# Kernel tuning notes

Measured on AMD Instinct MI355X. Metric: run time of the kernel, lower is better.

The kernel has to match this reference:

```python
import jax, jax.numpy as jnp
import numpy as np

# dims
B, C, H, W = 2, 256, 128, 256
P, G = 9, 8            # num_pts, num_groups
GC = C // G            # group_channels


def setup_inputs() -> dict:
    key = jax.random.key(0)
    ks = jax.random.split(key, 8)
    s = 0.02
    return {
        "feats1": jax.random.normal(ks[0], (B, C, H, W), jnp.float32),
        "feats2": jax.random.normal(ks[1], (B, C, H, W), jnp.float32),
        "anchor_points": jax.random.uniform(ks[2], (B, H * W, 2), jnp.float32),
        "norm1_g": jnp.ones((C,), jnp.float32), "norm1_b": jnp.zeros((C,), jnp.float32),
        "norm2_g": jnp.ones((C,), jnp.float32), "norm2_b": jnp.zeros((C,), jnp.float32),
        "Wv": jax.random.normal(ks[3], (C, C), jnp.float32) * s, "bv": jnp.zeros((C,), jnp.float32),
        "Ww": jax.random.normal(ks[4], (C, G * P), jnp.float32) * s, "bw": jnp.zeros((G * P,), jnp.float32),
        "Wk": jax.random.normal(ks[5], (C, P), jnp.float32) * s, "bk": jnp.zeros((P,), jnp.float32),
        "Wo": jax.random.normal(ks[6], (C, C), jnp.float32) * s, "bo": jnp.zeros((C,), jnp.float32),
    }


def _ln(x, g, b):
    # LayerNorm over the last (channel) axis, eps as torch default
    m = jnp.mean(x, axis=-1, keepdims=True)
    v = jnp.mean(jnp.square(x - m), axis=-1, keepdims=True)
    return (x - m) * jax.lax.rsqrt(v + 1e-5) * g + b


def _bilinear_sample(value, pts):
    # value: (b, H, W, C); pts: (b, N, 2) normalized [0,1] (x, y)
    # grid_sample semantics: align_corners=False, zero padding
    b, h, w, c = value.shape
    x = pts[..., 0] * w - 0.5
    y = pts[..., 1] * h - 0.5
    x0 = jnp.floor(x)
    y0 = jnp.floor(y)
    wx = (x - x0)[..., None]
    wy = (y - y0)[..., None]
    x0i = x0.astype(jnp.int32)
    y0i = y0.astype(jnp.int32)
    vflat = value.reshape(b, h * w, c)

    def gather(yi, xi):
        valid = (yi >= 0) & (yi < h) & (xi >= 0) & (xi < w)
        idx = jnp.clip(yi, 0, h - 1) * w + jnp.clip(xi, 0, w - 1)
        g = jnp.take_along_axis(vflat, idx[..., None], axis=1)
        return g * valid[..., None].astype(value.dtype)

    v00 = gather(y0i, x0i)
    v01 = gather(y0i, x0i + 1)
    v10 = gather(y0i + 1, x0i)
    v11 = gather(y0i + 1, x0i + 1)
    return (v00 * (1 - wx) * (1 - wy) + v01 * wx * (1 - wy)
            + v10 * (1 - wx) * wy + v11 * wx * wy)


def reference(feats1, feats2, anchor_points, norm1_g, norm1_b, norm2_g, norm2_b,
              Wv, bv, Ww, bw, Wk, bk, Wo, bo):
    b, c, h, w = feats1.shape
    hw = h * w
    # to_3d(dim=2): (b, c, h, w) -> (b, hw, c); LayerNorm over c
    x1 = _ln(feats1.reshape(b, c, hw).transpose(0, 2, 1), norm1_g, norm1_b)
    x2 = _ln(feats2.reshape(b, c, hw).transpose(0, 2, 1), norm2_g, norm2_b)

    # value_proj (1x1 conv == per-pixel linear)
    value = (x2 @ Wv + bv).reshape(b, h, w, c)

    # weight_proj -> (b, hw, P, G); channel layout p*G + g; softmax over the P points per group
    logits = (x1 @ Ww + bw).reshape(b, hw, P, G)
    wts = jax.nn.softmax(logits, axis=2)

    # 1D key-point generator: per-pixel learned offsets along x around the anchor
    off = x1 @ Wk + bk                                   # (b, hw, P) normalized offsets
    kx = anchor_points[..., 0:1] + off                   # (b, hw, P)
    ky = jnp.broadcast_to(anchor_points[..., 1:2], kx.shape)
    kp = jnp.stack([kx, ky], axis=-1)                    # (b, hw, P, 2)

    # deformable aggregation: bilinear gather + group-weighted sum over points
    samp = _bilinear_sample(value, kp.reshape(b, hw * P, 2)).reshape(b, hw, P, G, GC)
    agg = jnp.einsum('bnpgc,bnpg->bngc', samp, wts).reshape(b, hw, c)

    out = (agg @ Wo + bo).reshape(b, h, w, c).transpose(0, 3, 1, 2)  # (b, c, h, w)
    return out, kp.reshape(b, h, w, P, 2)
```

## Files before the change

### kernel.cpp

```cpp
#include <hip/hip_runtime.h>
#include <hip/hip_bf16.h>


constexpr int B = 2, C = 256, H = 128, W = 256;
constexpr int HW = H * W;
constexpr int P = 9, G = 8;
constexpr int PIX = 32;
constexpr int NPIX = B * HW;
constexpr int NBKT = 2 * 129;

typedef __attribute__((ext_vector_type(8))) __bf16 bf16x8;
typedef __attribute__((ext_vector_type(4))) float f32x4;
typedef __attribute__((ext_vector_type(2))) float f32x2;

static __device__ __forceinline__ unsigned short f2bf(float x) {
    __hip_bfloat16 h = __float2bfloat16(x);
    return *reinterpret_cast<unsigned short*>(&h);
}
static __device__ __forceinline__ unsigned int pack2(float a, float b) {
    return (unsigned int)f2bf(a) | ((unsigned int)f2bf(b) << 16);
}
static __device__ __forceinline__ float bf2f(unsigned short u) {
    return __uint_as_float((unsigned int)u << 16);
}
static __device__ __forceinline__ bf16x8 ldb8g(const unsigned short* p) {
    return *reinterpret_cast<const bf16x8*>(p);
}

__global__ __launch_bounds__(256) void k_prep(
    const float* __restrict__ Ww, const float* __restrict__ Wv,
    const float* __restrict__ Wo,
    unsigned short* __restrict__ WwT, unsigned short* __restrict__ WvT,
    unsigned short* __restrict__ WoT)
{
    int tid = blockIdx.x * 256 + threadIdx.x;
    if (tid < 20480) {
        int n = tid >> 8, k = tid & 255;
        WwT[tid] = f2bf((n < 72) ? Ww[k * 72 + n] : 0.f);
    } else if (tid < 20480 + 65536) {
        int i = tid - 20480;
        int n = i >> 8, k = i & 255;
        WvT[i] = f2bf(Wv[k * 256 + n]);
    } else {
        int i = tid - 86016;
        int n = i >> 8, k = i & 255;
        WoT[i] = f2bf(Wo[k * 256 + n]);
    }
}

static __device__ __forceinline__ int bucket_of(const float* anchor, int pix) {
    float ay = anchor[(size_t)pix * 2 + 1];
    int y0 = (int)floorf(ay * (float)H - 0.5f);
    y0 = min(max(y0, -1), H - 1);
    return (pix >> 15) * 129 + y0 + 1;
}

__global__ __launch_bounds__(1024) void k_hist(
    const float* __restrict__ anchor, int* __restrict__ hist64)
{
    __shared__ int h[NBKT];
    const int t = threadIdx.x, blk = blockIdx.x;
    for (int i = t; i < NBKT; i += 1024) h[i] = 0;
    __syncthreads();
    atomicAdd(&h[bucket_of(anchor, blk * 1024 + t)], 1);
    __syncthreads();
    for (int i = t; i < NBKT; i += 1024) hist64[blk * NBKT + i] = h[i];
}

__global__ __launch_bounds__(256) void k_scan(
    const int* __restrict__ hist64, int* __restrict__ off)
{
    __shared__ int tot[NBKT], base[NBKT];
    const int t = threadIdx.x;
    for (int bkt = t; bkt < NBKT; bkt += 256) {
        int run = 0;
        for (int blk = 0; blk < 64; ++blk) run += hist64[blk * NBKT + bkt];
        tot[bkt] = run;
    }
    __syncthreads();
    if (t == 0) {
        int run = 0;
        for (int i = 0; i < NBKT; ++i) { base[i] = run; run += tot[i]; }
    }
    __syncthreads();
    for (int bkt = t; bkt < NBKT; bkt += 256) {
        int run = base[bkt];
        for (int blk = 0; blk < 64; ++blk) {
            int v = hist64[blk * NBKT + bkt];
            off[blk * NBKT + bkt] = run;
            run += v;
        }
    }
}

__global__ __launch_bounds__(1024) void k_scatter(
    const float* __restrict__ anchor, const int* __restrict__ off,
    int* __restrict__ perm)
{
    __shared__ int cur[NBKT];
    const int t = threadIdx.x, blk = blockIdx.x;
    for (int i = t; i < NBKT; i += 1024) cur[i] = off[blk * NBKT + i];
    __syncthreads();
    int pix = blk * 1024 + t;
    int pos = atomicAdd(&cur[bucket_of(anchor, pix)], 1);
    perm[pos] = pix;
}

__global__ __launch_bounds__(256) void kA(
    const float* __restrict__ feats1, const float* __restrict__ anchor,
    const float* __restrict__ g1, const float* __restrict__ b1,
    const float* __restrict__ Wk, const float* __restrict__ bk,
    const unsigned short* __restrict__ WwT, const float* __restrict__ bw,
    unsigned short* __restrict__ wtsb, float* __restrict__ kp_out)
{
    __shared__ unsigned short Hi[PIX][264];
    __shared__ __align__(16) char smB[20480];
    __shared__ float meanA[PIX], rstdA[PIX], axL[PIX], ayL[PIX];

    float* WkL  = (float*)smB;
    float* red2 = (float*)(smB + 9216);
    float* red  = (float*)(smB + 18432);
    float* Lg   = (float*)smB;

    const int t = threadIdx.x;
    const int p = t & 31;
    const int part = t >> 5;
    const int gpix0 = blockIdx.x * PIX;
    const int b = gpix0 >> 15;
    const int n0 = gpix0 & (HW - 1);
    const float* Fb = feats1 + (size_t)b * C * HW;

    for (int i = t; i < 2304; i += 256) WkL[i] = Wk[i];
    if (t < PIX) {
        axL[t] = anchor[((size_t)gpix0 + t) * 2 + 0];
        ayL[t] = anchor[((size_t)gpix0 + t) * 2 + 1];
    }

    float x[32];
    #pragma unroll
    for (int i = 0; i < 32; ++i)
        x[i] = Fb[(size_t)(part * 32 + i) * HW + n0 + p];

    float s = 0.f, ss = 0.f;
    #pragma unroll
    for (int i = 0; i < 32; ++i) { s += x[i]; ss += x[i] * x[i]; }
    red[part * 32 + p] = s;
    red[256 + part * 32 + p] = ss;
    __syncthreads();
    if (part == 0) {
        float s2 = 0.f, ss2 = 0.f;
        #pragma unroll
        for (int k = 0; k < 8; ++k) { s2 += red[k * 32 + p]; ss2 += red[256 + k * 32 + p]; }
        float mean = s2 * (1.f / C);
        float var  = ss2 * (1.f / C) - mean * mean;
        meanA[p] = mean; rstdA[p] = rsqrtf(var + 1e-5f);
    }
    __syncthreads();

    {
        float mean = meanA[p], rstd = rstdA[p];
        #pragma unroll
        for (int i = 0; i < 32; ++i) {
            int c = part * 32 + i;
            x[i] = (x[i] - mean) * rstd * g1[c] + b1[c];
        }
    }

    {
        float po[9];
        #pragma unroll
        for (int pt = 0; pt < 9; ++pt) po[pt] = 0.f;
        #pragma unroll 4
        for (int i = 0; i < 32; ++i) {
            int c = part * 32 + i;
            float xv = x[i];
            #pragma unroll
            for (int pt = 0; pt < 9; ++pt) po[pt] += xv * WkL[c * 9 + pt];
        }
        #pragma unroll
        for (int pt = 0; pt < 9; ++pt) red2[(part * 32 + p) * 9 + pt] = po[pt];
    }

    {
        unsigned int* row = (unsigned int*)&Hi[p][part * 32];
        #pragma unroll
        for (int i = 0; i < 16; ++i) row[i] = pack2(x[2 * i], x[2 * i + 1]);
    }
    __syncthreads();

    for (int tau = t; tau < 288; tau += 256) {
        int px = tau & 31, pt = tau >> 5;
        float offv = bk[pt];
        #pragma unroll
        for (int k = 0; k < 8; ++k) offv += red2[(k * 32 + px) * 9 + pt];
        size_t o = (((size_t)gpix0 + px) * P + pt) * 2;
        kp_out[o] = axL[px] + offv;
        kp_out[o + 1] = ayL[px];
    }

    const int wave = t >> 6, lane = t & 63;
    const int l15 = lane & 15, quad = lane >> 4;
    const int mt = wave & 1;
    const int ntb = (wave >> 1) * 3;
    const int ntc = (wave >> 1) ? 2 : 3;

    f32x4 acc[3];
    #pragma unroll
    for (int j = 0; j < 3; ++j) acc[j] = (f32x4){0.f, 0.f, 0.f, 0.f};

    const unsigned short* arow = &Hi[mt * 16 + l15][quad * 8];
    for (int kk = 0; kk < 8; ++kk) {
        bf16x8 a = *reinterpret_cast<const bf16x8*>(arow + kk * 32);
        for (int j = 0; j < 3; ++j) {
            if (j < ntc) {
                bf16x8 bfr = ldb8g(WwT + (size_t)((ntb + j) * 16 + l15) * 256 + quad * 8 + kk * 32);
                acc[j] = __builtin_amdgcn_mfma_f32_16x16x32_bf16(a, bfr, acc[j], 0, 0, 0);
            }
        }
    }
    __syncthreads();

    #pragma unroll
    for (int j = 0; j < 3; ++j) {
        if (j < ntc) {
            int n = (ntb + j) * 16 + l15;
            if (n < 72) {
                float bwn = bw[n];
                #pragma unroll
                for (int r = 0; r < 4; ++r)
                    Lg[(mt * 16 + quad * 4 + r) * 81 + n] = acc[j][r] + bwn;
            }
        }
    }
    __syncthreads();

    {
        int px = t >> 3, g = t & 7;
        float m = -1e30f;
        #pragma unroll
        for (int pt = 0; pt < P; ++pt) m = fmaxf(m, Lg[px * 81 + pt * 8 + g]);
        float e[P], sum = 0.f;
        #pragma unroll
        for (int pt = 0; pt < P; ++pt) { e[pt] = __expf(Lg[px * 81 + pt * 8 + g] - m); sum += e[pt]; }
        float inv = 1.f / sum;
        unsigned short* wb = wtsb + ((size_t)gpix0 + px) * 72 + g * 9;
        #pragma unroll
        for (int pt = 0; pt < P; ++pt) wb[pt] = f2bf(e[pt] * inv);
    }
}

__global__ __launch_bounds__(256) void kB(
    const float* __restrict__ feats2,
    const float* __restrict__ g2, const float* __restrict__ b2,
    const unsigned short* __restrict__ WvT, const float* __restrict__ bv,
    unsigned short* __restrict__ val)
{
    __shared__ unsigned short Hi[PIX][264];
    __shared__ float red[2][8][PIX];
    __shared__ float meanA[PIX], rstdA[PIX];

    const int t = threadIdx.x;
    const int p = t & 31;
    const int part = t >> 5;
    const int gpix0 = blockIdx.x * PIX;
    const int b = gpix0 >> 15;
    const int n0 = gpix0 & (HW - 1);
    const float* Fb = feats2 + (size_t)b * C * HW;

    float x[32];
    #pragma unroll
    for (int i = 0; i < 32; ++i)
        x[i] = Fb[(size_t)(part * 32 + i) * HW + n0 + p];

    float s = 0.f, ss = 0.f;
    #pragma unroll
    for (int i = 0; i < 32; ++i) { s += x[i]; ss += x[i] * x[i]; }
    red[0][part][p] = s; red[1][part][p] = ss;
    __syncthreads();
    if (part == 0) {
        float s2 = 0.f, ss2 = 0.f;
        #pragma unroll
        for (int k = 0; k < 8; ++k) { s2 += red[0][k][p]; ss2 += red[1][k][p]; }
        float mean = s2 * (1.f / C);
        float var  = ss2 * (1.f / C) - mean * mean;
        meanA[p] = mean; rstdA[p] = rsqrtf(var + 1e-5f);
    }
    __syncthreads();
    {
        float mean = meanA[p], rstd = rstdA[p];
        unsigned int* row = (unsigned int*)&Hi[p][part * 32];
        #pragma unroll
        for (int i = 0; i < 16; ++i) {
            float v0 = (x[2 * i] - mean) * rstd * g2[part * 32 + 2 * i] + b2[part * 32 + 2 * i];
            float v1 = (x[2 * i + 1] - mean) * rstd * g2[part * 32 + 2 * i + 1] + b2[part * 32 + 2 * i + 1];
            row[i] = pack2(v0, v1);
        }
    }
    __syncthreads();

    const int wave = t >> 6, lane = t & 63;
    const int l15 = lane & 15, quad = lane >> 4;
    const int m0 = wave * 64;

    f32x4 acc[4][2];
    #pragma unroll
    for (int ms = 0; ms < 4; ++ms)
        #pragma unroll
        for (int nt = 0; nt < 2; ++nt)
            acc[ms][nt] = (f32x4){0.f, 0.f, 0.f, 0.f};

    for (int kk = 0; kk < 8; ++kk) {
        bf16x8 a[4], bfr[2];
        #pragma unroll
        for (int ms = 0; ms < 4; ++ms)
            a[ms] = ldb8g(WvT + (size_t)(m0 + ms * 16 + l15) * 256 + quad * 8 + kk * 32);
        #pragma unroll
        for (int nt = 0; nt < 2; ++nt)
            bfr[nt] = *reinterpret_cast<const bf16x8*>(&Hi[nt * 16 + l15][quad * 8 + kk * 32]);
        #pragma unroll
        for (int ms = 0; ms < 4; ++ms)
            #pragma unroll
            for (int nt = 0; nt < 2; ++nt)
                acc[ms][nt] = __builtin_amdgcn_mfma_f32_16x16x32_bf16(a[ms], bfr[nt], acc[ms][nt], 0, 0, 0);
    }

    #pragma unroll
    for (int ms = 0; ms < 4; ++ms) {
        int ch0 = m0 + ms * 16 + quad * 4;
        float b0 = bv[ch0], b1v = bv[ch0 + 1], b2v = bv[ch0 + 2], b3 = bv[ch0 + 3];
        #pragma unroll
        for (int nt = 0; nt < 2; ++nt) {
            int pix = gpix0 + nt * 16 + l15;
            uint2 o;
            o.x = pack2(acc[ms][nt][0] + b0, acc[ms][nt][1] + b1v);
            o.y = pack2(acc[ms][nt][2] + b2v, acc[ms][nt][3] + b3);
            *reinterpret_cast<uint2*>(val + (size_t)pix * 256 + ch0) = o;
        }
    }
}

__global__ __launch_bounds__(256) void k_gather(
    const unsigned short* __restrict__ wtsb,
    const float* __restrict__ kp,
    const unsigned short* __restrict__ val,
    const int* __restrict__ perm,
    unsigned short* __restrict__ aggb)
{
    __shared__ float Wl[PIX][72];
    __shared__ float KPl[PIX][18];
    __shared__ int pixL[PIX];

    const int t = threadIdx.x;
    const int phys = blockIdx.x;
    const int lb = (phys & 7) * 256 + (phys >> 3);
    const int gpix0 = lb * PIX;

    if (t < PIX) pixL[t] = perm[gpix0 + t];
    __syncthreads();

    {
        int px = t >> 3, j = t & 7;
        int pix = pixL[px];
        const unsigned short* wrow = wtsb + (size_t)pix * 72 + j * 9;
        #pragma unroll
        for (int k = 0; k < 9; ++k) Wl[px][j * 9 + k] = bf2f(wrow[k]);
        const float* krow = kp + (size_t)pix * 18;
        for (int k = j; k < 18; k += 8) KPl[px][k] = krow[k];
    }
    __syncthreads();

    const int wave = t >> 6, lane = t & 63;
    const int gl = lane >> 3;

    for (int px = wave; px < PIX; px += 4) {
        const int pix = pixL[px];
        const unsigned short* vbp = val + ((size_t)(pix >> 15) * HW) * 256 + 4 * lane;

        const float ay = KPl[px][1];
        float yf = ay * (float)H - 0.5f;
        float y0f = floorf(yf);
        float wy = yf - y0f;
        int y0 = (int)y0f;
        float e0 = (((unsigned)y0 < (unsigned)H) ? 1.f : 0.f) * (1.f - wy);
        float e1 = (((unsigned)(y0 + 1) < (unsigned)H) ? 1.f : 0.f) * wy;
        int yb0 = min(max(y0, 0), H - 1) * W;
        int yb1 = min(max(y0 + 1, 0), H - 1) * W;

        f32x2 a01 = (f32x2){0.f, 0.f};
        f32x2 a23 = (f32x2){0.f, 0.f};

        #pragma unroll
        for (int pt = 0; pt < P; ++pt) {
            float kx = KPl[px][2 * pt];
            float w  = Wl[px][gl * 9 + pt];
            float xf = kx * (float)W - 0.5f;
            float x0f = floorf(xf);
            float wx = xf - x0f;
            int x0 = (int)x0f;
            float t0 = w * (1.f - wx) * (((unsigned)x0 < (unsigned)W) ? 1.f : 0.f);
            float t1 = w * wx * (((unsigned)(x0 + 1) < (unsigned)W) ? 1.f : 0.f);
            int x0c = min(max(x0, 0), W - 1);
            int x1c = min(max(x0 + 1, 0), W - 1);

            float c00 = t0 * e0, c01 = t1 * e0, c10 = t0 * e1, c11 = t1 * e1;

            uint2 u00 = *(const uint2*)(vbp + ((size_t)(yb0 + x0c) << 8));
            uint2 u01 = *(const uint2*)(vbp + ((size_t)(yb0 + x1c) << 8));
            uint2 u10 = *(const uint2*)(vbp + ((size_t)(yb1 + x0c) << 8));
            uint2 u11 = *(const uint2*)(vbp + ((size_t)(yb1 + x1c) << 8));

            f32x2 v;
            v.x = __uint_as_float(u00.x << 16); v.y = __uint_as_float(u00.x & 0xffff0000u);
            a01 += v * c00;
            v.x = __uint_as_float(u00.y << 16); v.y = __uint_as_float(u00.y & 0xffff0000u);
            a23 += v * c00;
            v.x = __uint_as_float(u01.x << 16); v.y = __uint_as_float(u01.x & 0xffff0000u);
            a01 += v * c01;
            v.x = __uint_as_float(u01.y << 16); v.y = __uint_as_float(u01.y & 0xffff0000u);
            a23 += v * c01;
            v.x = __uint_as_float(u10.x << 16); v.y = __uint_as_float(u10.x & 0xffff0000u);
            a01 += v * c10;
            v.x = __uint_as_float(u10.y << 16); v.y = __uint_as_float(u10.y & 0xffff0000u);
            a23 += v * c10;
            v.x = __uint_as_float(u11.x << 16); v.y = __uint_as_float(u11.x & 0xffff0000u);
            a01 += v * c11;
            v.x = __uint_as_float(u11.y << 16); v.y = __uint_as_float(u11.y & 0xffff0000u);
            a23 += v * c11;
        }

        uint2 o;
        o.x = pack2(a01.x, a01.y);
        o.y = pack2(a23.x, a23.y);
        *reinterpret_cast<uint2*>(aggb + ((size_t)pix << 8) + 4 * lane) = o;
    }
}

__global__ __launch_bounds__(256) void k_gemmo(
    const unsigned short* __restrict__ aggb,
    const unsigned short* __restrict__ WoT,
    const float* __restrict__ bo,
    float* __restrict__ out)
{
    const int t = threadIdx.x;
    const int wave = t >> 6, lane = t & 63;
    const int n_base = blockIdx.x * 64;
    const int b = n_base >> 15;
    const int hw0 = n_base & (HW - 1);
    const int m0 = wave * 64;
    const int l15 = lane & 15, quad = lane >> 4;

    f32x4 acc[4][4];
    #pragma unroll
    for (int ms = 0; ms < 4; ++ms)
        #pragma unroll
        for (int ns = 0; ns < 4; ++ns)
            acc[ms][ns] = (f32x4){0.f, 0.f, 0.f, 0.f};

    size_t aoff[4], boff[4];
    #pragma unroll
    for (int ms = 0; ms < 4; ++ms)
        aoff[ms] = (size_t)(m0 + ms * 16 + l15) * 256 + quad * 8;
    #pragma unroll
    for (int ns = 0; ns < 4; ++ns)
        boff[ns] = (size_t)(n_base + ns * 16 + l15) * 256 + quad * 8;

    for (int kk = 0; kk < 8; ++kk) {
        bf16x8 a[4], bfr[4];
        #pragma unroll
        for (int ms = 0; ms < 4; ++ms) a[ms] = ldb8g(WoT + aoff[ms] + kk * 32);
        #pragma unroll
        for (int ns = 0; ns < 4; ++ns) bfr[ns] = ldb8g(aggb + boff[ns] + kk * 32);
        #pragma unroll
        for (int ms = 0; ms < 4; ++ms)
            #pragma unroll
            for (int ns = 0; ns < 4; ++ns)
                acc[ms][ns] = __builtin_amdgcn_mfma_f32_16x16x32_bf16(a[ms], bfr[ns], acc[ms][ns], 0, 0, 0);
    }

    float bor[4][4];
    #pragma unroll
    for (int ms = 0; ms < 4; ++ms)
        #pragma unroll
        for (int r = 0; r < 4; ++r)
            bor[ms][r] = bo[m0 + ms * 16 + quad * 4 + r];

    #pragma unroll
    for (int ms = 0; ms < 4; ++ms) {
        #pragma unroll
        for (int ns = 0; ns < 4; ++ns) {
            #pragma unroll
            for (int r = 0; r < 4; ++r) {
                int ch = m0 + ms * 16 + quad * 4 + r;
                out[((size_t)b * 256 + ch) * HW + hw0 + ns * 16 + l15] = acc[ms][ns][r] + bor[ms][r];
            }
        }
    }
}

extern "C" void kernel_launch(void* const* d_in, const int* in_sizes, int n_in,
                              void* d_out, int out_size, void* d_ws, size_t ws_size,
                              hipStream_t stream)
{
    const float* feats1 = (const float*)d_in[0];
    const float* feats2 = (const float*)d_in[1];
    const float* anchor = (const float*)d_in[2];
    const float* n1g    = (const float*)d_in[3];
    const float* n1b    = (const float*)d_in[4];
    const float* n2g    = (const float*)d_in[5];
    const float* n2b    = (const float*)d_in[6];
    const float* Wv     = (const float*)d_in[7];
    const float* bv     = (const float*)d_in[8];
    const float* Ww     = (const float*)d_in[9];
    const float* bw     = (const float*)d_in[10];
    const float* Wk     = (const float*)d_in[11];
    const float* bk     = (const float*)d_in[12];
    const float* Wo     = (const float*)d_in[13];
    const float* bo     = (const float*)d_in[14];

    float* out = (float*)d_out;
    float* kp  = out + (size_t)B * C * HW;

    char* ws = (char*)d_ws;
    unsigned short* val  = (unsigned short*)(ws);
    unsigned short* aggb = (unsigned short*)(ws + 33554432);
    unsigned short* wtsb = (unsigned short*)(ws + 67108864);
    unsigned short* WwT  = (unsigned short*)(ws + 76546048);
    unsigned short* WvT  = (unsigned short*)(ws + 76587008);
    unsigned short* WoT  = (unsigned short*)(ws + 76718080);
    int* perm   = (int*)(ws + 76849152);
    int* hist64 = (int*)(ws + 77111296);
    int* off    = (int*)(ws + 77375488);

    k_prep   <<<592,  256,  0, stream>>>(Ww, Wv, Wo, WwT, WvT, WoT);
    k_hist   <<<64,   1024, 0, stream>>>(anchor, hist64);
    k_scan   <<<1,    256,  0, stream>>>(hist64, off);
    k_scatter<<<64,   1024, 0, stream>>>(anchor, off, perm);
    kA       <<<2048, 256,  0, stream>>>(feats1, anchor, n1g, n1b, Wk, bk, WwT, bw, wtsb, kp);
    kB       <<<2048, 256,  0, stream>>>(feats2, n2g, n2b, WvT, bv, val);
    k_gather <<<2048, 256,  0, stream>>>(wtsb, kp, val, perm, aggb);
    k_gemmo  <<<1024, 256,  0, stream>>>(aggb, WoT, bo, out);
}
```

Baseline: 409.0 us.

## Store value tensor in fp16 and precompute bilinear coefficients per block

The value projection now writes fp16 instead of bf16, and the gather kernel accumulates with v_fma_mix_f32, which converts each fp16 half and does the multiply-add in one instruction, replacing separate unpack plus FMA. Bilinear corner weights and row/column byte offsets are computed once per (pixel, point) into shared memory. Each wave then broadcasts them with readlane instead of every lane recomputing floor, clamp and validity logic. This lowers ALU work in the gather loop. The risks are fp16 range and precision on the value tensor, plus reliance on inline assembly.

New measurement: 403.3 us. About the same (-1.4%).

```diff
diff --git a/kernel.cpp b/kernel.cpp
--- a/kernel.cpp
+++ b/kernel.cpp
@@ -12,6 +12,7 @@
 typedef __attribute__((ext_vector_type(8))) __bf16 bf16x8;
 typedef __attribute__((ext_vector_type(4))) float f32x4;
 typedef __attribute__((ext_vector_type(2))) float f32x2;
+typedef __attribute__((ext_vector_type(2))) __fp16 fp16x2;
 
 static __device__ __forceinline__ unsigned short f2bf(float x) {
     __hip_bfloat16 h = __float2bfloat16(x);
@@ -20,12 +21,23 @@
 static __device__ __forceinline__ unsigned int pack2(float a, float b) {
     return (unsigned int)f2bf(a) | ((unsigned int)f2bf(b) << 16);
 }
+static __device__ __forceinline__ unsigned int pkh(float a, float b) {
+    fp16x2 h = __builtin_amdgcn_cvt_pkrtz(a, b);
+    return *reinterpret_cast<unsigned int*>(&h);
+}
 static __device__ __forceinline__ float bf2f(unsigned short u) {
     return __uint_as_float((unsigned int)u << 16);
 }
 static __device__ __forceinline__ bf16x8 ldb8g(const unsigned short* p) {
     return *reinterpret_cast<const bf16x8*>(p);
 }
+
+#define FMA_LO(acc, pk, c) \
+    asm("v_fma_mix_f32 %0, %1, %2, %0 op_sel:[0,0,0] op_sel_hi:[1,0,0]" \
+        : "+v"(acc) : "v"(pk), "v"(c))
+#define FMA_HI(acc, pk, c) \
+    asm("v_fma_mix_f32 %0, %1, %2, %0 op_sel:[1,0,0] op_sel_hi:[1,0,0]" \
+        : "+v"(acc) : "v"(pk), "v"(c))
 
 __global__ __launch_bounds__(256) void k_prep(
     const float* __restrict__ Ww, const float* __restrict__ Wv,
@@ -332,8 +344,8 @@
         for (int nt = 0; nt < 2; ++nt) {
             int pix = gpix0 + nt * 16 + l15;
             uint2 o;
-            o.x = pack2(acc[ms][nt][0] + b0, acc[ms][nt][1] + b1v);
-            o.y = pack2(acc[ms][nt][2] + b2v, acc[ms][nt][3] + b3);
+            o.x = pkh(acc[ms][nt][0] + b0, acc[ms][nt][1] + b1v);
+            o.y = pkh(acc[ms][nt][2] + b2v, acc[ms][nt][3] + b3);
             *reinterpret_cast<uint2*>(val + (size_t)pix * 256 + ch0) = o;
         }
     }
@@ -346,8 +358,9 @@
     const int* __restrict__ perm,
     unsigned short* __restrict__ aggb)
 {
-    __shared__ float Wl[PIX][72];
-    __shared__ float KPl[PIX][18];
+    __shared__ int   CF[PIX][64];
+    __shared__ float WL[PIX * 8 * 10];
+    __shared__ float EY[PIX][2];
     __shared__ int pixL[PIX];
 
     const int t = threadIdx.x;
@@ -355,82 +368,96 @@
     const int lb = (phys & 7) * 256 + (phys >> 3);
     const int gpix0 = lb * PIX;
 
-    if (t < PIX) pixL[t] = perm[gpix0 + t];
-    __syncthreads();
-
+    if (t < PIX) {
+        int pix = perm[gpix0 + t];
+        pixL[t] = pix;
+        float ay = kp[(size_t)pix * 18 + 1];
+        float yf = ay * (float)H - 0.5f;
+        float y0f = floorf(yf);
+        float wy = yf - y0f;
+        int y0 = (int)y0f;
+        EY[t][0] = (((unsigned)y0 < (unsigned)H) ? 1.f : 0.f) * (1.f - wy);
+        EY[t][1] = (((unsigned)(y0 + 1) < (unsigned)H) ? 1.f : 0.f) * wy;
+        int yb0 = min(max(y0, 0), H - 1) * W;
+        int yb1 = min(max(y0 + 1, 0), H - 1) * W;
+        int base = (pix >> 15) * HW;
+        CF[t][54] = (base + yb0) << 9;
+        CF[t][55] = (base + yb1) << 9;
+    }
+    __syncthreads();
+
+    for (int tau = t; tau < 288; tau += 256) {
+        int px = tau & 31, pt = tau >> 5;
+        int pix = pixL[px];
+        float kx = kp[(size_t)pix * 18 + 2 * pt];
+        float e0 = EY[px][0], e1 = EY[px][1];
+        float xf = kx * (float)W - 0.5f;
+        float x0f = floorf(xf);
+        float wx = xf - x0f;
+        int x0 = (int)x0f;
+        float g0 = (1.f - wx) * (((unsigned)x0 < (unsigned)W) ? 1.f : 0.f);
+        float g1v = wx * (((unsigned)(x0 + 1) < (unsigned)W) ? 1.f : 0.f);
+        CF[px][pt * 6 + 0] = __float_as_int(g0 * e0);
+        CF[px][pt * 6 + 1] = __float_as_int(g1v * e0);
+        CF[px][pt * 6 + 2] = __float_as_int(g0 * e1);
+        CF[px][pt * 6 + 3] = __float_as_int(g1v * e1);
+        CF[px][pt * 6 + 4] = min(max(x0, 0), W - 1) << 9;
+        CF[px][pt * 6 + 5] = min(max(x0 + 1, 0), W - 1) << 9;
+    }
     {
         int px = t >> 3, j = t & 7;
         int pix = pixL[px];
         const unsigned short* wrow = wtsb + (size_t)pix * 72 + j * 9;
-        #pragma unroll
-        for (int k = 0; k < 9; ++k) Wl[px][j * 9 + k] = bf2f(wrow[k]);
-        const float* krow = kp + (size_t)pix * 18;
-        for (int k = j; k < 18; k += 8) KPl[px][k] = krow[k];
+        float* wl = &WL[(px * 8 + j) * 10];
+        #pragma unroll
+        for (int k = 0; k < 9; ++k) wl[k] = bf2f(wrow[k]);
     }
     __syncthreads();
 
     const int wave = t >> 6, lane = t & 63;
     const int gl = lane >> 3;
+    const char* vb = (const char*)val;
 
     for (int px = wave; px < PIX; px += 4) {
-        const int pix = pixL[px];
-        const unsigned short* vbp = val + ((size_t)(pix >> 15) * HW) * 256 + 4 * lane;
-
-        const float ay = KPl[px][1];
-        float yf = ay * (float)H - 0.5f;
-        float y0f = floorf(yf);
-        float wy = yf - y0f;
-        int y0 = (int)y0f;
-        float e0 = (((unsigned)y0 < (unsigned)H) ? 1.f : 0.f) * (1.f - wy);
-        float e1 = (((unsigned)(y0 + 1) < (unsigned)H) ? 1.f : 0.f) * wy;
-        int yb0 = min(max(y0, 0), H - 1) * W;
-        int yb1 = min(max(y0 + 1, 0), H - 1) * W;
-
-        f32x2 a01 = (f32x2){0.f, 0.f};
-        f32x2 a23 = (f32x2){0.f, 0.f};
+        int cw = CF[px][lane];
+        unsigned rb0 = (unsigned)__builtin_amdgcn_readlane(cw, 54);
+        unsigned rb1 = (unsigned)__builtin_amdgcn_readlane(cw, 55);
+        unsigned lb0 = rb0 + (unsigned)lane * 8u;
+        unsigned lb1 = rb1 + (unsigned)lane * 8u;
+        const float* wl = &WL[(px * 8 + gl) * 10];
+
+        float a0 = 0.f, a1 = 0.f, a2 = 0.f, a3 = 0.f;
 
         #pragma unroll
         for (int pt = 0; pt < P; ++pt) {
-            float kx = KPl[px][2 * pt];
-            float w  = Wl[px][gl * 9 + pt];
-            float xf = kx * (float)W - 0.5f;
-            float x0f = floorf(xf);
-            float wx = xf - x0f;
-            int x0 = (int)x0f;
-            float t0 = w * (1.f - wx) * (((unsigned)x0 < (unsigned)W) ? 1.f : 0.f);
-            float t1 = w * wx * (((unsigned)(x0 + 1) < (unsigned)W) ? 1.f : 0.f);
-            int x0c = min(max(x0, 0), W - 1);
-            int x1c = min(max(x0 + 1, 0), W - 1);
-
-            float c00 = t0 * e0, c01 = t1 * e0, c10 = t0 * e1, c11 = t1 * e1;
-
-            uint2 u00 = *(const uint2*)(vbp + ((size_t)(yb0 + x0c) << 8));
-            uint2 u01 = *(const uint2*)(vbp + ((size_t)(yb0 + x1c) << 8));
-            uint2 u10 = *(const uint2*)(vbp + ((size_t)(yb1 + x0c) << 8));
-            uint2 u11 = *(const uint2*)(vbp + ((size_t)(yb1 + x1c) << 8));
-
-            f32x2 v;
-            v.x = __uint_as_float(u00.x << 16); v.y = __uint_as_float(u00.x & 0xffff0000u);
-            a01 += v * c00;
-            v.x = __uint_as_float(u00.y << 16); v.y = __uint_as_float(u00.y & 0xffff0000u);
-            a23 += v * c00;
-            v.x = __uint_as_float(u01.x << 16); v.y = __uint_as_float(u01.x & 0xffff0000u);
-            a01 += v * c01;
-            v.x = __uint_as_float(u01.y << 16); v.y = __uint_as_float(u01.y & 0xffff0000u);
-            a23 += v * c01;
-            v.x = __uint_as_float(u10.x << 16); v.y = __uint_as_float(u10.x & 0xffff0000u);
-            a01 += v * c10;
-            v.x = __uint_as_float(u10.y << 16); v.y = __uint_as_float(u10.y & 0xffff0000u);
-            a23 += v * c10;
-            v.x = __uint_as_float(u11.x << 16); v.y = __uint_as_float(u11.x & 0xffff0000u);
-            a01 += v * c11;
-            v.x = __uint_as_float(u11.y << 16); v.y = __uint_as_float(u11.y & 0xffff0000u);
-            a23 += v * c11;
-        }
-
+            float u00 = __int_as_float(__builtin_amdgcn_readlane(cw, pt * 6 + 0));
+            float u01 = __int_as_float(__builtin_amdgcn_readlane(cw, pt * 6 + 1));
+            float u10 = __int_as_float(__builtin_amdgcn_readlane(cw, pt * 6 + 2));
+            float u11 = __int_as_float(__builtin_amdgcn_readlane(cw, pt * 6 + 3));
+            unsigned xb0 = (unsigned)__builtin_amdgcn_readlane(cw, pt * 6 + 4);
+            unsigned xb1 = (unsigned)__builtin_amdgcn_readlane(cw, pt * 6 + 5);
+            float w = wl[pt];
+            float c00 = w * u00, c01 = w * u01, c10 = w * u10, c11 = w * u11;
+
+            uint2 q00 = *(const uint2*)(vb + (lb0 + xb0));
+            uint2 q01 = *(const uint2*)(vb + (lb0 + xb1));
+            uint2 q10 = *(const uint2*)(vb + (lb1 + xb0));
+            uint2 q11 = *(const uint2*)(vb + (lb1 + xb1));
+
+            FMA_LO(a0, q00.x, c00); FMA_HI(a1, q00.x, c00);
+            FMA_LO(a2, q00.y, c00); FMA_HI(a3, q00.y, c00);
+            FMA_LO(a0, q01.x, c01); FMA_HI(a1, q01.x, c01);
+            FMA_LO(a2, q01.y, c01); FMA_HI(a3, q01.y, c01);
+            FMA_LO(a0, q10.x, c10); FMA_HI(a1, q10.x, c10);
+            FMA_LO(a2, q10.y, c10); FMA_HI(a3, q10.y, c10);
+            FMA_LO(a0, q11.x, c11); FMA_HI(a1, q11.x, c11);
+            FMA_LO(a2, q11.y, c11); FMA_HI(a3, q11.y, c11);
+        }
+
+        int pix = pixL[px];
         uint2 o;
-        o.x = pack2(a01.x, a01.y);
-        o.y = pack2(a23.x, a23.y);
+        o.x = pack2(a0, a1);
+        o.y = pack2(a2, a3);
         *reinterpret_cast<uint2*>(aggb + ((size_t)pix << 8) + 4 * lane) = o;
     }
 }
```
